# Kernel optimization log

Hardware: AMD Instinct MI355X
Metric: run time of the kernel (lower is better)

The kernel has to match this reference:

```python
import jax, jax.numpy as jnp
import numpy as np

N = 1_000_000
FEAT_DIM = 256
N_CLASS = 345
N_DOMAIN = 6
BETA = 0.5
EPS = 1e-5


def setup_inputs() -> dict:
    key = jax.random.key(0)
    k1, k2, k3, k4 = jax.random.split(key, 4)
    feats = jax.random.normal(k1, (N, FEAT_DIM), dtype=jnp.float32)
    mean = jax.random.normal(k2, (N_DOMAIN, N_CLASS, FEAT_DIM), dtype=jnp.float32)
    amount = jnp.zeros((N_DOMAIN, N_CLASS), dtype=jnp.float32)
    labels = jax.random.randint(k3, (N,), 0, N_CLASS, dtype=jnp.int64 if jax.config.jax_enable_x64 else jnp.int32)
    domains = jax.random.randint(k4, (N,), 0, N_DOMAIN, dtype=jnp.int64 if jax.config.jax_enable_x64 else jnp.int32)
    return {"feats": feats, "mean": mean, "amount": amount,
            "labels": labels, "domains": domains}


def reference(feats, mean, amount, labels, domains):
    # Segmented per-(domain, class) mean of feats. Equivalent to the original
    # onehot broadcast-multiply + sum, but without the O(N*C*F) intermediate.
    seg = domains * N_CLASS + labels  # [N]
    sums = jax.ops.segment_sum(feats, seg, num_segments=N_DOMAIN * N_CLASS)
    sums = sums.reshape(N_DOMAIN, N_CLASS, FEAT_DIM)
    counts = jax.ops.segment_sum(jnp.ones((feats.shape[0],), dtype=feats.dtype), seg,
                                 num_segments=N_DOMAIN * N_CLASS)
    counts = counts.reshape(N_DOMAIN, N_CLASS)

    tmp_mean = sums / (counts[..., None] + EPS)  # [D, C, F]
    # Mask of (domain, class) cells actually observed (tmp_mean row nonzero)
    tmp_mask = (jnp.sum(tmp_mean, axis=-1) != 0).astype(feats.dtype)[..., None]  # [D, C, 1]

    new_mean = mean * (1.0 - tmp_mask) + (mean * BETA + tmp_mean * (1.0 - BETA)) * tmp_mask
    new_amount = jnp.where(counts > 0, jnp.ones_like(amount), amount)
    return new_mean, new_amount
```

## Files before the change

### kernel.cpp

```cpp
#include <hip/hip_runtime.h>
#include <stddef.h>

constexpr int FEAT = 256;
constexpr int F4   = FEAT / 4;
constexpr int NCLS = 345;
constexpr int NDOM = 6;
constexpr int NSEG = NCLS * NDOM;
constexpr int SB   = 256;
constexpr float BETA = 0.5f;
constexpr float EPS  = 1e-5f;

__global__ void __launch_bounds__(256)
k_seg_hist(const int* __restrict__ labels, const int* __restrict__ domains,
           int n, int chunk, int* __restrict__ seg, int* __restrict__ W) {
    __shared__ int h[NSEG];
    for (int i = threadIdx.x; i < NSEG; i += blockDim.x) h[i] = 0;
    __syncthreads();
    const int b  = blockIdx.x;
    const int lo = b * chunk;
    const int hi = min(n, lo + chunk);
    for (int i = lo + threadIdx.x; i < hi; i += blockDim.x) {
        int s = domains[i] * NCLS + labels[i];
        seg[i] = s;
        atomicAdd(&h[s], 1);
    }
    __syncthreads();
    int* Wb = W + (size_t)b * NSEG;
    for (int i = threadIdx.x; i < NSEG; i += blockDim.x) Wb[i] = h[i];
}

__global__ void k_totals(const int* __restrict__ W, int* __restrict__ totals) {
    const int s = blockIdx.x;
    const int t = threadIdx.x;
    int sum = 0;
    for (int b = t; b < SB; b += 64) sum += W[(size_t)b * NSEG + s];
    for (int off = 1; off < 64; off <<= 1) sum += __shfl_xor(sum, off, 64);
    if (t == 0) totals[s] = sum;
}

__global__ void k_scan(const int* __restrict__ totals, int* __restrict__ offsets) {
    constexpr int T  = 256;
    constexpr int CH = (NSEG + T - 1) / T;
    __shared__ int csum[T];
    int t = threadIdx.x;
    int base = t * CH;
    int sum = 0;
    for (int j = 0; j < CH; ++j) {
        int idx = base + j;
        if (idx < NSEG) sum += totals[idx];
    }
    csum[t] = sum;
    __syncthreads();
    for (int off = 1; off < T; off <<= 1) {
        int v = (t >= off) ? csum[t - off] : 0;
        __syncthreads();
        csum[t] += v;
        __syncthreads();
    }
    int run = csum[t] - sum;
    for (int j = 0; j < CH; ++j) {
        int idx = base + j;
        if (idx < NSEG) {
            offsets[idx] = run;
            run += totals[idx];
        }
    }
}

__global__ void __launch_bounds__(256)
k_bases(const int* __restrict__ W, const int* __restrict__ offsets,
        int* __restrict__ Bmat) {
    const int s = blockIdx.x;
    const int t = threadIdx.x;
    __shared__ int sc[SB];
    int w = W[(size_t)t * NSEG + s];
    sc[t] = w;
    __syncthreads();
    for (int off = 1; off < SB; off <<= 1) {
        int v = (t >= off) ? sc[t - off] : 0;
        __syncthreads();
        sc[t] += v;
        __syncthreads();
    }
    Bmat[(size_t)t * NSEG + s] = offsets[s] + (sc[t] - w);
}

__global__ void __launch_bounds__(256)
k_scatter(const int* __restrict__ seg, int n, int chunk,
          const int* __restrict__ Bmat, int* __restrict__ sorted) {
    __shared__ int cur[NSEG];
    const int b = blockIdx.x;
    const int* Bb = Bmat + (size_t)b * NSEG;
    for (int i = threadIdx.x; i < NSEG; i += blockDim.x) cur[i] = Bb[i];
    __syncthreads();
    const int lo = b * chunk;
    const int hi = min(n, lo + chunk);
    for (int i = lo + threadIdx.x; i < hi; i += blockDim.x) {
        int s = seg[i];
        int pos = atomicAdd(&cur[s], 1);
        sorted[pos] = i;
    }
}

__global__ void __launch_bounds__(256)
k_reduce(const float* __restrict__ feats, const float* __restrict__ mean,
         const float* __restrict__ amount, const int* __restrict__ sorted,
         const int* __restrict__ counts, const int* __restrict__ offsets,
         float* __restrict__ out) {
    const int seg  = blockIdx.x;
    const int cnt  = counts[seg];
    const int base = offsets[seg];
    const int lane = threadIdx.x & 63;
    const int rp   = threadIdx.x >> 6;

    float4 acc = make_float4(0.f, 0.f, 0.f, 0.f);
    int r = rp;
    for (; r + 28 < cnt; r += 32) {
        int i0 = sorted[base + r];
        int i1 = sorted[base + r + 4];
        int i2 = sorted[base + r + 8];
        int i3 = sorted[base + r + 12];
        int i4 = sorted[base + r + 16];
        int i5 = sorted[base + r + 20];
        int i6 = sorted[base + r + 24];
        int i7 = sorted[base + r + 28];
        float4 v0 = reinterpret_cast<const float4*>(feats + (size_t)i0 * FEAT)[lane];
        float4 v1 = reinterpret_cast<const float4*>(feats + (size_t)i1 * FEAT)[lane];
        float4 v2 = reinterpret_cast<const float4*>(feats + (size_t)i2 * FEAT)[lane];
        float4 v3 = reinterpret_cast<const float4*>(feats + (size_t)i3 * FEAT)[lane];
        float4 v4 = reinterpret_cast<const float4*>(feats + (size_t)i4 * FEAT)[lane];
        float4 v5 = reinterpret_cast<const float4*>(feats + (size_t)i5 * FEAT)[lane];
        float4 v6 = reinterpret_cast<const float4*>(feats + (size_t)i6 * FEAT)[lane];
        float4 v7 = reinterpret_cast<const float4*>(feats + (size_t)i7 * FEAT)[lane];
        acc.x += (v0.x + v1.x) + (v2.x + v3.x) + (v4.x + v5.x) + (v6.x + v7.x);
        acc.y += (v0.y + v1.y) + (v2.y + v3.y) + (v4.y + v5.y) + (v6.y + v7.y);
        acc.z += (v0.z + v1.z) + (v2.z + v3.z) + (v4.z + v5.z) + (v6.z + v7.z);
        acc.w += (v0.w + v1.w) + (v2.w + v3.w) + (v4.w + v5.w) + (v6.w + v7.w);
    }
    for (; r < cnt; r += 4) {
        int i0 = sorted[base + r];
        float4 v0 = reinterpret_cast<const float4*>(feats + (size_t)i0 * FEAT)[lane];
        acc.x += v0.x; acc.y += v0.y; acc.z += v0.z; acc.w += v0.w;
    }

    __shared__ float4 sh[4][F4];
    sh[rp][lane] = acc;
    __syncthreads();
    if (rp == 0) {
        float4 s = acc;
        float4 b = sh[1][lane]; s.x += b.x; s.y += b.y; s.z += b.z; s.w += b.w;
        b = sh[2][lane];        s.x += b.x; s.y += b.y; s.z += b.z; s.w += b.w;
        b = sh[3][lane];        s.x += b.x; s.y += b.y; s.z += b.z; s.w += b.w;

        float inv = 1.0f / ((float)cnt + EPS);
        float4 tm = make_float4(s.x * inv, s.y * inv, s.z * inv, s.w * inv);

        float lsum = tm.x + tm.y + tm.z + tm.w;
        for (int off = 1; off < 64; off <<= 1) lsum += __shfl_xor(lsum, off, 64);
        bool msk = (lsum != 0.0f);

        float4 m4 = reinterpret_cast<const float4*>(mean)[(size_t)seg * F4 + lane];
        float4 o;
        if (msk) {
            o.x = m4.x * BETA + tm.x * (1.f - BETA);
            o.y = m4.y * BETA + tm.y * (1.f - BETA);
            o.z = m4.z * BETA + tm.z * (1.f - BETA);
            o.w = m4.w * BETA + tm.w * (1.f - BETA);
        } else {
            o = m4;
        }
        reinterpret_cast<float4*>(out)[(size_t)seg * F4 + lane] = o;
        if (lane == 0) {
            out[(size_t)NSEG * FEAT + seg] = (cnt > 0) ? 1.0f : amount[seg];
        }
    }
}

__global__ void k_fb_zero(float* __restrict__ out, int total) {
    int stride = gridDim.x * blockDim.x;
    for (int i = blockIdx.x * blockDim.x + threadIdx.x; i < total; i += stride) out[i] = 0.f;
}

__global__ void k_fb_acc(const float* __restrict__ feats, const int* __restrict__ labels,
                         const int* __restrict__ domains, int n, float* __restrict__ out) {
    int lane   = threadIdx.x & 63;
    int gwave  = (blockIdx.x * blockDim.x + threadIdx.x) >> 6;
    int nwaves = (gridDim.x * blockDim.x) >> 6;
    for (int i = gwave; i < n; i += nwaves) {
        int seg = domains[i] * NCLS + labels[i];
        float4 v = reinterpret_cast<const float4*>(feats + (size_t)i * FEAT)[lane];
        float* dst = out + (size_t)seg * FEAT + lane * 4;
        atomicAdd(dst + 0, v.x);
        atomicAdd(dst + 1, v.y);
        atomicAdd(dst + 2, v.z);
        atomicAdd(dst + 3, v.w);
        if (lane == 0) atomicAdd(out + (size_t)NSEG * FEAT + seg, 1.0f);
    }
}

__global__ void k_fb_epi(const float* __restrict__ mean, const float* __restrict__ amount,
                         float* __restrict__ out) {
    int seg  = blockIdx.x;
    int lane = threadIdx.x;
    float cntf = out[(size_t)NSEG * FEAT + seg];
    float4 s = reinterpret_cast<float4*>(out)[(size_t)seg * F4 + lane];
    float inv = 1.0f / (cntf + EPS);
    float4 tm = make_float4(s.x * inv, s.y * inv, s.z * inv, s.w * inv);
    float lsum = tm.x + tm.y + tm.z + tm.w;
    for (int off = 1; off < 64; off <<= 1) lsum += __shfl_xor(lsum, off, 64);
    bool msk = (lsum != 0.0f);
    float4 m4 = reinterpret_cast<const float4*>(mean)[(size_t)seg * F4 + lane];
    float4 o;
    if (msk) {
        o.x = m4.x * BETA + tm.x * (1.f - BETA);
        o.y = m4.y * BETA + tm.y * (1.f - BETA);
        o.z = m4.z * BETA + tm.z * (1.f - BETA);
        o.w = m4.w * BETA + tm.w * (1.f - BETA);
    } else {
        o = m4;
    }
    reinterpret_cast<float4*>(out)[(size_t)seg * F4 + lane] = o;
    if (lane == 0) {
        out[(size_t)NSEG * FEAT + seg] = (cntf > 0.5f) ? 1.0f : amount[seg];
    }
}

extern "C" void kernel_launch(void* const* d_in, const int* in_sizes, int n_in,
                              void* d_out, int out_size, void* d_ws, size_t ws_size,
                              hipStream_t stream) {
    const float* feats   = (const float*)d_in[0];
    const float* mean    = (const float*)d_in[1];
    const float* amount  = (const float*)d_in[2];
    const int*   labels  = (const int*)d_in[3];
    const int*   domains = (const int*)d_in[4];
    float* out = (float*)d_out;
    const int n = in_sizes[3];
    const int chunk = (n + SB - 1) / SB;

    size_t need = ((size_t)n * 2 + (size_t)SB * NSEG * 2 + (size_t)NSEG * 2) * sizeof(int);
    if (ws_size >= need) {
        int* seg     = (int*)d_ws;
        int* W       = seg + n;
        int* totals  = W + (size_t)SB * NSEG;
        int* offsets = totals + NSEG;
        int* Bmat    = offsets + NSEG;
        int* sorted  = Bmat + (size_t)SB * NSEG;

        k_seg_hist<<<SB, 256, 0, stream>>>(labels, domains, n, chunk, seg, W);
        k_totals<<<NSEG, 64, 0, stream>>>(W, totals);
        k_scan<<<1, 256, 0, stream>>>(totals, offsets);
        k_bases<<<NSEG, 256, 0, stream>>>(W, offsets, Bmat);
        k_scatter<<<SB, 256, 0, stream>>>(seg, n, chunk, Bmat, sorted);
        k_reduce<<<NSEG, 256, 0, stream>>>(feats, mean, amount, sorted, totals, offsets, out);
    } else {
        int total = NSEG * FEAT + NSEG;
        k_fb_zero<<<(total + 255) / 256, 256, 0, stream>>>(out, total);
        k_fb_acc<<<2048, 256, 0, stream>>>(feats, labels, domains, n, out);
        k_fb_epi<<<NSEG, 64, 0, stream>>>(mean, amount, out);
    }
}
```

Measured before the change: 242.8 us.

## Use persistent work-stealing blocks with LDS-staged indices and nontemporal loads in reduce

The segmented reduce kernel becomes persistent: 2048 blocks pull segment ids from a global ticket counter, which k_scan resets, instead of launching one block per segment. Sorted row indices are staged into shared memory in tiles of 1024 before the gather. Feature rows are read with nontemporal loads to avoid polluting cache with the 1 GB stream. This adds an atomic and extra barriers per segment, and each segment is still handled by a single block, so per-segment parallelism is unchanged.

```diff
diff --git a/kernel.cpp b/kernel.cpp
--- a/kernel.cpp
+++ b/kernel.cpp
@@ -7,8 +7,11 @@
 constexpr int NDOM = 6;
 constexpr int NSEG = NCLS * NDOM;
 constexpr int SB   = 256;
+constexpr int ITILE = 1024;
 constexpr float BETA = 0.5f;
 constexpr float EPS  = 1e-5f;
+
+typedef float f32x4 __attribute__((ext_vector_type(4)));
 
 __global__ void __launch_bounds__(256)
 k_seg_hist(const int* __restrict__ labels, const int* __restrict__ domains,
@@ -38,11 +41,13 @@
     if (t == 0) totals[s] = sum;
 }
 
-__global__ void k_scan(const int* __restrict__ totals, int* __restrict__ offsets) {
+__global__ void k_scan(const int* __restrict__ totals, int* __restrict__ offsets,
+                       int* __restrict__ ticket) {
     constexpr int T  = 256;
     constexpr int CH = (NSEG + T - 1) / T;
     __shared__ int csum[T];
     int t = threadIdx.x;
+    if (t == 0) ticket[0] = 0;
     int base = t * CH;
     int sum = 0;
     for (int j = 0; j < CH; ++j) {
@@ -106,73 +111,68 @@
 k_reduce(const float* __restrict__ feats, const float* __restrict__ mean,
          const float* __restrict__ amount, const int* __restrict__ sorted,
          const int* __restrict__ counts, const int* __restrict__ offsets,
-         float* __restrict__ out) {
-    const int seg  = blockIdx.x;
-    const int cnt  = counts[seg];
-    const int base = offsets[seg];
+         int* __restrict__ ticket, float* __restrict__ out) {
+    __shared__ int   idx[ITILE];
+    __shared__ f32x4 sh[4][F4];
+    __shared__ int   s_seg;
     const int lane = threadIdx.x & 63;
     const int rp   = threadIdx.x >> 6;
 
-    float4 acc = make_float4(0.f, 0.f, 0.f, 0.f);
-    int r = rp;
-    for (; r + 28 < cnt; r += 32) {
-        int i0 = sorted[base + r];
-        int i1 = sorted[base + r + 4];
-        int i2 = sorted[base + r + 8];
-        int i3 = sorted[base + r + 12];
-        int i4 = sorted[base + r + 16];
-        int i5 = sorted[base + r + 20];
-        int i6 = sorted[base + r + 24];
-        int i7 = sorted[base + r + 28];
-        float4 v0 = reinterpret_cast<const float4*>(feats + (size_t)i0 * FEAT)[lane];
-        float4 v1 = reinterpret_cast<const float4*>(feats + (size_t)i1 * FEAT)[lane];
-        float4 v2 = reinterpret_cast<const float4*>(feats + (size_t)i2 * FEAT)[lane];
-        float4 v3 = reinterpret_cast<const float4*>(feats + (size_t)i3 * FEAT)[lane];
-        float4 v4 = reinterpret_cast<const float4*>(feats + (size_t)i4 * FEAT)[lane];
-        float4 v5 = reinterpret_cast<const float4*>(feats + (size_t)i5 * FEAT)[lane];
-        float4 v6 = reinterpret_cast<const float4*>(feats + (size_t)i6 * FEAT)[lane];
-        float4 v7 = reinterpret_cast<const float4*>(feats + (size_t)i7 * FEAT)[lane];
-        acc.x += (v0.x + v1.x) + (v2.x + v3.x) + (v4.x + v5.x) + (v6.x + v7.x);
-        acc.y += (v0.y + v1.y) + (v2.y + v3.y) + (v4.y + v5.y) + (v6.y + v7.y);
-        acc.z += (v0.z + v1.z) + (v2.z + v3.z) + (v4.z + v5.z) + (v6.z + v7.z);
-        acc.w += (v0.w + v1.w) + (v2.w + v3.w) + (v4.w + v5.w) + (v6.w + v7.w);
-    }
-    for (; r < cnt; r += 4) {
-        int i0 = sorted[base + r];
-        float4 v0 = reinterpret_cast<const float4*>(feats + (size_t)i0 * FEAT)[lane];
-        acc.x += v0.x; acc.y += v0.y; acc.z += v0.z; acc.w += v0.w;
-    }
-
-    __shared__ float4 sh[4][F4];
-    sh[rp][lane] = acc;
-    __syncthreads();
-    if (rp == 0) {
-        float4 s = acc;
-        float4 b = sh[1][lane]; s.x += b.x; s.y += b.y; s.z += b.z; s.w += b.w;
-        b = sh[2][lane];        s.x += b.x; s.y += b.y; s.z += b.z; s.w += b.w;
-        b = sh[3][lane];        s.x += b.x; s.y += b.y; s.z += b.z; s.w += b.w;
-
-        float inv = 1.0f / ((float)cnt + EPS);
-        float4 tm = make_float4(s.x * inv, s.y * inv, s.z * inv, s.w * inv);
-
-        float lsum = tm.x + tm.y + tm.z + tm.w;
-        for (int off = 1; off < 64; off <<= 1) lsum += __shfl_xor(lsum, off, 64);
-        bool msk = (lsum != 0.0f);
-
-        float4 m4 = reinterpret_cast<const float4*>(mean)[(size_t)seg * F4 + lane];
-        float4 o;
-        if (msk) {
-            o.x = m4.x * BETA + tm.x * (1.f - BETA);
-            o.y = m4.y * BETA + tm.y * (1.f - BETA);
-            o.z = m4.z * BETA + tm.z * (1.f - BETA);
-            o.w = m4.w * BETA + tm.w * (1.f - BETA);
-        } else {
-            o = m4;
+    for (;;) {
+        if (threadIdx.x == 0) s_seg = atomicAdd(ticket, 1);
+        __syncthreads();
+        const int seg = s_seg;
+        if (seg >= NSEG) break;
+        const int cnt  = counts[seg];
+        const int base = offsets[seg];
+
+        f32x4 acc = (f32x4)0.0f;
+        for (int t0 = 0; t0 < cnt; t0 += ITILE) {
+            const int tile = min(ITILE, cnt - t0);
+            for (int i = threadIdx.x; i < tile; i += 256) idx[i] = sorted[base + t0 + i];
+            __syncthreads();
+            int r = rp;
+            for (; r + 28 < tile; r += 32) {
+                int i0 = idx[r];      int i1 = idx[r + 4];
+                int i2 = idx[r + 8];  int i3 = idx[r + 12];
+                int i4 = idx[r + 16]; int i5 = idx[r + 20];
+                int i6 = idx[r + 24]; int i7 = idx[r + 28];
+                f32x4 v0 = __builtin_nontemporal_load(reinterpret_cast<const f32x4*>(feats + (size_t)i0 * FEAT) + lane);
+                f32x4 v1 = __builtin_nontemporal_load(reinterpret_cast<const f32x4*>(feats + (size_t)i1 * FEAT) + lane);
+                f32x4 v2 = __builtin_nontemporal_load(reinterpret_cast<const f32x4*>(feats + (size_t)i2 * FEAT) + lane);
+                f32x4 v3 = __builtin_nontemporal_load(reinterpret_cast<const f32x4*>(feats + (size_t)i3 * FEAT) + lane);
+                f32x4 v4 = __builtin_nontemporal_load(reinterpret_cast<const f32x4*>(feats + (size_t)i4 * FEAT) + lane);
+                f32x4 v5 = __builtin_nontemporal_load(reinterpret_cast<const f32x4*>(feats + (size_t)i5 * FEAT) + lane);
+                f32x4 v6 = __builtin_nontemporal_load(reinterpret_cast<const f32x4*>(feats + (size_t)i6 * FEAT) + lane);
+                f32x4 v7 = __builtin_nontemporal_load(reinterpret_cast<const f32x4*>(feats + (size_t)i7 * FEAT) + lane);
+                acc += (v0 + v1) + (v2 + v3) + ((v4 + v5) + (v6 + v7));
+            }
+            for (; r < tile; r += 4) {
+                int i0 = idx[r];
+                acc += __builtin_nontemporal_load(reinterpret_cast<const f32x4*>(feats + (size_t)i0 * FEAT) + lane);
+            }
+            __syncthreads();
         }
-        reinterpret_cast<float4*>(out)[(size_t)seg * F4 + lane] = o;
-        if (lane == 0) {
-            out[(size_t)NSEG * FEAT + seg] = (cnt > 0) ? 1.0f : amount[seg];
+
+        sh[rp][lane] = acc;
+        __syncthreads();
+        if (rp == 0) {
+            f32x4 s = acc + sh[1][lane] + sh[2][lane] + sh[3][lane];
+            float inv = 1.0f / ((float)cnt + EPS);
+            f32x4 tm = s * inv;
+
+            float lsum = tm.x + tm.y + tm.z + tm.w;
+            for (int off = 1; off < 64; off <<= 1) lsum += __shfl_xor(lsum, off, 64);
+            bool msk = (lsum != 0.0f);
+
+            f32x4 m4 = reinterpret_cast<const f32x4*>(mean)[(size_t)seg * F4 + lane];
+            f32x4 o = msk ? (m4 * BETA + tm * (1.0f - BETA)) : m4;
+            reinterpret_cast<f32x4*>(out)[(size_t)seg * F4 + lane] = o;
+            if (lane == 0) {
+                out[(size_t)NSEG * FEAT + seg] = (cnt > 0) ? 1.0f : amount[seg];
+            }
         }
+        __syncthreads();
     }
 }
 
@@ -188,7 +188,7 @@
     int nwaves = (gridDim.x * blockDim.x) >> 6;
     for (int i = gwave; i < n; i += nwaves) {
         int seg = domains[i] * NCLS + labels[i];
-        float4 v = reinterpret_cast<const float4*>(feats + (size_t)i * FEAT)[lane];
+        const float4 v = reinterpret_cast<const float4*>(feats + (size_t)i * FEAT)[lane];
         float* dst = out + (size_t)seg * FEAT + lane * 4;
         atomicAdd(dst + 0, v.x);
         atomicAdd(dst + 1, v.y);
@@ -237,7 +237,7 @@
     const int n = in_sizes[3];
     const int chunk = (n + SB - 1) / SB;
 
-    size_t need = ((size_t)n * 2 + (size_t)SB * NSEG * 2 + (size_t)NSEG * 2) * sizeof(int);
+    size_t need = ((size_t)n * 2 + (size_t)SB * NSEG * 2 + (size_t)NSEG * 2 + 1) * sizeof(int);
     if (ws_size >= need) {
         int* seg     = (int*)d_ws;
         int* W       = seg + n;
@@ -245,13 +245,14 @@
         int* offsets = totals + NSEG;
         int* Bmat    = offsets + NSEG;
         int* sorted  = Bmat + (size_t)SB * NSEG;
+        int* ticket  = sorted + n;
 
         k_seg_hist<<<SB, 256, 0, stream>>>(labels, domains, n, chunk, seg, W);
         k_totals<<<NSEG, 64, 0, stream>>>(W, totals);
-        k_scan<<<1, 256, 0, stream>>>(totals, offsets);
+        k_scan<<<1, 256, 0, stream>>>(totals, offsets, ticket);
         k_bases<<<NSEG, 256, 0, stream>>>(W, offsets, Bmat);
         k_scatter<<<SB, 256, 0, stream>>>(seg, n, chunk, Bmat, sorted);
-        k_reduce<<<NSEG, 256, 0, stream>>>(feats, mean, amount, sorted, totals, offsets, out);
+        k_reduce<<<2048, 256, 0, stream>>>(feats, mean, amount, sorted, totals, offsets, ticket, out);
     } else {
         int total = NSEG * FEAT + NSEG;
         k_fb_zero<<<(total + 255) / 256, 256, 0, stream>>>(out, total);
```

Result: no change. 246.9 us (+1.7%).
